# Performance work log

Hardware: AMD Instinct MI355X
Metric: run time of the kernel (lower is better)

The kernel has to match this reference:

```python
import jax, jax.numpy as jnp
import numpy as np

B, CIN, COUT, H, W, K = 4, 64, 64, 128, 128, 3
KK = K * K


def setup_inputs() -> dict:
    key = jax.random.key(0)
    k1, k2, k3, k4 = jax.random.split(key, 4)
    x = jax.random.normal(k1, (B, CIN, H, W), dtype=jnp.float32)
    offset = jax.random.normal(k2, (B, 2 * KK, H, W), dtype=jnp.float32)
    mask = jax.random.uniform(k3, (B, KK, H, W), dtype=jnp.float32)
    n = CIN * KK
    stdv = 1.0 / np.sqrt(n)
    weight = jax.random.uniform(k4, (COUT, CIN, K, K), dtype=jnp.float32,
                                minval=-stdv, maxval=stdv)
    bias = jnp.zeros((COUT,), dtype=jnp.float32)
    return {"x": x, "offset": offset, "mask": mask, "weight": weight, "bias": bias}


def _sample(x, ci, cj):
    # x: (b,c,h,w); ci,cj: (b,h,w,kk) int32 -> (b,c,h,w,kk), zero outside bounds
    b, c, h, w = x.shape
    valid = (ci >= 0) & (ci < h) & (cj >= 0) & (cj < w)  # (b,h,w,kk)
    idx = jnp.clip(ci, 0, h - 1) * w + jnp.clip(cj, 0, w - 1)
    flat = x.reshape(b, c, h * w)
    g = jnp.take_along_axis(flat, idx.reshape(b, 1, -1), axis=2)
    g = g.reshape(b, c, h, w, -1)
    return jnp.where(valid[:, None], g, jnp.zeros((), x.dtype))


def reference(x, offset, mask, weight, bias):
    b, c, h, w = x.shape
    # offset: (b, kk*2, h, w) -> (b, h, w, kk, 2)
    off = offset.reshape(b, KK, 2, h, w).transpose(0, 3, 4, 1, 2)
    # base sampling grid: coord[i,j,ki,kj] = (i-1+ki, j-1+kj), flattened over kk
    di, dj = jnp.meshgrid(jnp.arange(-(K // 2), K // 2 + 1),
                          jnp.arange(-(K // 2), K // 2 + 1), indexing='ij')
    base_i = jnp.arange(h, dtype=jnp.float32)[:, None, None] + di.reshape(1, 1, KK)
    base_j = jnp.arange(w, dtype=jnp.float32)[None, :, None] + dj.reshape(1, 1, KK)
    coord_i = off[..., 0] + base_i  # (b,h,w,kk)
    coord_j = off[..., 1] + base_j

    lt_i = jnp.floor(coord_i)
    lt_j = jnp.floor(coord_j)
    rb_i = jnp.ceil(coord_i)
    rb_j = jnp.ceil(coord_j)
    li, lj = lt_i.astype(jnp.int32), lt_j.astype(jnp.int32)
    ri, rj = rb_i.astype(jnp.int32), rb_j.astype(jnp.int32)

    v_lt = _sample(x, li, lj)
    v_rb = _sample(x, ri, rj)
    v_rt = _sample(x, li, rj)
    v_lb = _sample(x, ri, lj)

    # bilinear fractions, broadcast over channel dim
    fi = (coord_i - lt_i)[:, None]  # (b,1,h,w,kk)
    fj = (coord_j - lt_j)[:, None]
    v_t = v_lt + fj * (v_rt - v_lt)
    v_b = v_lb + fj * (v_rb - v_lb)
    v = v_t + fi * (v_b - v_t)  # (b,c,h,w,kk)

    # modulation mask: (b,kk,h,w) -> (b,1,h,w,kk)
    v = v * mask.transpose(0, 2, 3, 1)[:, None]

    w_flat = weight.reshape(weight.shape[0], c, KK)
    out = jnp.einsum('oik,bihwk->bohw', w_flat, v)
    return out + bias[None, :, None, None]
```

## Files before the change

kernel.cpp:

```cpp
#include <hip/hip_runtime.h>

#define B_   4
#define CIN  64
#define COUT 64
#define H_   128
#define W_   128
#define HW   (H_*W_)
#define KK   9
#define PIX  (B_*H_*W_)
#define R_   4
#define REG  16
#define NBLK 1024

typedef short bf16x8 __attribute__((ext_vector_type(8)));
typedef float f32x4  __attribute__((ext_vector_type(4)));
typedef float f32x2  __attribute__((ext_vector_type(2)));
typedef unsigned int u32;
typedef unsigned int u32x4 __attribute__((ext_vector_type(4)));

__device__ __forceinline__ unsigned short f2bf(float f) {
    unsigned int u = __float_as_uint(f);
    u = (u + 0x7FFFu + ((u >> 16) & 1u)) >> 16;
    return (unsigned short)u;
}

__global__ __launch_bounds__(256) void k_transpose(const float* __restrict__ x,
                                                   unsigned short* __restrict__ xt) {
    __shared__ float lds[64 * 129];
    int bi = blockIdx.x;
    int b = bi >> 7, i = bi & 127;
    int tid = threadIdx.x;
#pragma unroll
    for (int cc = 0; cc < 32; ++cc) {
        int c = cc * 2 + (tid >> 7);
        int w = tid & 127;
        lds[c * 129 + w] = x[((b * CIN + c) * H_ + i) * W_ + w];
    }
    __syncthreads();
#pragma unroll
    for (int q = 0; q < 32; ++q) {
        int c = tid & 63;
        int w = q * 4 + (tid >> 6);
        xt[((b * H_ + i) * W_ + w) * CIN + c] = f2bf(lds[c * 129 + w]);
    }
}

__global__ __launch_bounds__(256) void k_weight(const float* __restrict__ w,
                                                unsigned short* __restrict__ wtf) {
    int t = blockIdx.x * 256 + threadIdx.x;
    if (t >= 18 * 4 * 64 * 8) return;
    int j    = t & 7;
    int lane = (t >> 3) & 63;
    int nt   = (t >> 9) & 3;
    int s    = t >> 11;
    int kg   = s * 32 + ((lane >> 4) << 3) + j;
    int n    = nt * 16 + (lane & 15);
    int kpos = kg >> 6, c = kg & 63;
    wtf[t] = f2bf(w[(n * CIN + c) * 9 + kpos]);
}

__global__ __launch_bounds__(256, 4) void k_main(
    const unsigned short* __restrict__ xt,
    const float* __restrict__ offset,
    const float* __restrict__ mask,
    const unsigned short* __restrict__ wtf,
    const float* __restrict__ bias,
    float* __restrict__ out) {
    __shared__ __align__(16) unsigned char smem[REG * REG * 128];

    const int tid  = threadIdx.x;
    const int lane = tid & 63;
    const int wv   = tid >> 6;
    const int T  = ((blockIdx.x & 7) << 7) + (blockIdx.x >> 3);
    const int b  = T >> 8;
    const int i0 = ((T >> 4) & 15) * 8;
    const int j0 = (T & 15) * 8;
    const char* xb = (const char*)xt + (size_t)b * HW * 128;

    {
        const int iA = i0 - R_, jA = j0 - R_;
#pragma unroll
        for (int k = 0; k < 8; ++k) {
            int linear = k * 256 + tid;
            int rec = linear >> 3, c = linear & 7;
            int gr = min(max(iA + (rec >> 4), 0), H_ - 1);
            int gc = min(max(jA + (rec & 15), 0), W_ - 1);
            u32x4 v = *(const u32x4*)(xb + ((gr * W_ + gc) << 7) + (c << 4));
            *(u32x4*)(smem + (rec << 7) + (((c + rec) & 7) << 4)) = v;
        }
    }
    __syncthreads();

    const int p  = lane & 15;
    const int g  = lane >> 4;
    const int ir = i0 + wv * 2 + (p >> 3);
    const int jc = j0 + (p & 7);
    const float* offp = offset + (size_t)b * 18 * HW + ir * W_ + jc;
    const float* mskp = mask   + (size_t)b * 9  * HW + ir * W_ + jc;
    const bf16x8* wp  = (const bf16x8*)wtf;

    f32x4 acc0 = {0,0,0,0}, acc1 = {0,0,0,0}, acc2 = {0,0,0,0}, acc3 = {0,0,0,0};

#pragma unroll
    for (int kp = 0; kp < 9; ++kp) {
        float oi  = offp[(2 * kp) * HW];
        float oj  = offp[(2 * kp + 1) * HW];
        float msk = mskp[kp * HW];
        float ci = oi + (float)(ir + kp / 3 - 1);
        float cj = oj + (float)(jc + kp % 3 - 1);
        float fli = floorf(ci), flj = floorf(cj);
        float fi = ci - fli, fj = cj - flj;
        int li = (int)fli, lj = (int)flj;
        int li1 = li + 1, lj1 = lj + 1;
        float vy0 = (li  >= 0 && li  < H_) ? 1.f : 0.f;
        float vy1 = (li1 >= 0 && li1 < H_) ? 1.f : 0.f;
        float vx0 = (lj  >= 0 && lj  < W_) ? 1.f : 0.f;
        float vx1 = (lj1 >= 0 && lj1 < W_) ? 1.f : 0.f;
        float gi = fi * msk, gj = fj * msk;
        float w11 = gi * fj;
        f32x4 w4;
        w4.x = (msk - gi - gj + w11) * vy0 * vx0;
        w4.y = (gj - w11) * vy0 * vx1;
        w4.z = (gi - w11) * vy1 * vx0;
        w4.w = w11 * vy1 * vx1;
        int y0 = min(max(li,  0), H_ - 1), y1 = min(max(li1, 0), H_ - 1);
        int x0 = min(max(lj,  0), W_ - 1), x1 = min(max(lj1, 0), W_ - 1);
        int a00 = (y0 * W_ + x0) << 7, a01 = (y0 * W_ + x1) << 7;
        int a10 = (y1 * W_ + x0) << 7, a11 = (y1 * W_ + x1) << 7;
        int rli = li - (i0 - R_), rlj = lj - (j0 - R_);
        bool inr = ((unsigned)rli <= 14u) && ((unsigned)rlj <= 14u);
        int rli_c = min(max(rli, 0), 14), rlj_c = min(max(rlj, 0), 14);
        int r00 = rli_c * 16 + rlj_c;
        int r01 = r00 + 1, r10 = r00 + 16, r11 = r00 + 17;

#pragma unroll
        for (int h = 0; h < 2; ++h) {
            int ch = h * 4 + g;
            u32x4 q00 = *(const u32x4*)(smem + (r00 << 7) + (((ch + r00) & 7) << 4));
            u32x4 q01 = *(const u32x4*)(smem + (r01 << 7) + (((ch + r01) & 7) << 4));
            u32x4 q10 = *(const u32x4*)(smem + (r10 << 7) + (((ch + r10) & 7) << 4));
            u32x4 q11 = *(const u32x4*)(smem + (r11 << 7) + (((ch + r11) & 7) << 4));
            if (!inr) {
                int c = (g << 4) + (h << 6);
                q00 = *(const u32x4*)(xb + a00 + c);
                q01 = *(const u32x4*)(xb + a01 + c);
                q10 = *(const u32x4*)(xb + a10 + c);
                q11 = *(const u32x4*)(xb + a11 + c);
            }
            f32x2 wx = {w4.x, w4.x}, wy = {w4.y, w4.y};
            f32x2 wz = {w4.z, w4.z}, ww = {w4.w, w4.w};
            u32x4 po;
#pragma unroll
            for (int q = 0; q < 4; ++q) {
                f32x2 c00 = {__uint_as_float(q00[q] << 16), __uint_as_float(q00[q] & 0xFFFF0000u)};
                f32x2 c01 = {__uint_as_float(q01[q] << 16), __uint_as_float(q01[q] & 0xFFFF0000u)};
                f32x2 c10 = {__uint_as_float(q10[q] << 16), __uint_as_float(q10[q] & 0xFFFF0000u)};
                f32x2 c11 = {__uint_as_float(q11[q] << 16), __uint_as_float(q11[q] & 0xFFFF0000u)};
                f32x2 r = wx * c00 + wy * c01 + wz * c10 + ww * c11;
                po[q] = __builtin_amdgcn_perm(__float_as_uint(r.y) + 0x8000u,
                                              __float_as_uint(r.x) + 0x8000u, 0x07060302u);
            }
            bf16x8 af; *(u32x4*)&af = po;
            int s = kp * 2 + h;
            acc0 = __builtin_amdgcn_mfma_f32_16x16x32_bf16(af, wp[(s*4+0)*64 + lane], acc0, 0, 0, 0);
            acc1 = __builtin_amdgcn_mfma_f32_16x16x32_bf16(af, wp[(s*4+1)*64 + lane], acc1, 0, 0, 0);
            acc2 = __builtin_amdgcn_mfma_f32_16x16x32_bf16(af, wp[(s*4+2)*64 + lane], acc2, 0, 0, 0);
            acc3 = __builtin_amdgcn_mfma_f32_16x16x32_bf16(af, wp[(s*4+3)*64 + lane], acc3, 0, 0, 0);
        }
    }

    __syncthreads();
    float* cst = (float*)smem;
    {
        f32x4 v0 = acc0, v1 = acc1, v2 = acc2, v3 = acc3;
        float bs0 = bias[p], bs1 = bias[16 + p], bs2 = bias[32 + p], bs3 = bias[48 + p];
#pragma unroll
        for (int r = 0; r < 4; ++r) { v0[r] += bs0; v1[r] += bs1; v2[r] += bs2; v3[r] += bs3; }
        const int pm = wv * 16 + (g << 2);
        *(f32x4*)&cst[(p)      * 68 + pm] = v0;
        *(f32x4*)&cst[(16 + p) * 68 + pm] = v1;
        *(f32x4*)&cst[(32 + p) * 68 + pm] = v2;
        *(f32x4*)&cst[(48 + p) * 68 + pm] = v3;
    }
    __syncthreads();
    const int cl  = tid >> 4;
    const int px4 = (tid & 15) * 4;
    const size_t obase = (size_t)b * (COUT * HW) + (i0 + (px4 >> 3)) * W_ + j0 + (px4 & 7);
#pragma unroll
    for (int c4 = 0; c4 < 4; ++c4) {
        int cout = c4 * 16 + cl;
        f32x4 vv = *(const f32x4*)&cst[cout * 68 + px4];
        __builtin_nontemporal_store(vv, (f32x4*)&out[obase + (size_t)cout * HW]);
    }
}

extern "C" void kernel_launch(void* const* d_in, const int* in_sizes, int n_in,
                              void* d_out, int out_size, void* d_ws, size_t ws_size,
                              hipStream_t stream) {
    const float* x      = (const float*)d_in[0];
    const float* offset = (const float*)d_in[1];
    const float* mask   = (const float*)d_in[2];
    const float* weight = (const float*)d_in[3];
    const float* bias   = (const float*)d_in[4];
    float* out = (float*)d_out;
    unsigned short* xt  = (unsigned short*)d_ws;
    unsigned short* wtf = xt + (size_t)B_ * H_ * W_ * CIN;

    k_transpose<<<B_ * H_, 256, 0, stream>>>(x, xt);
    k_weight<<<144, 256, 0, stream>>>(weight, wtf);
    k_main<<<NBLK, 256, 0, stream>>>(xt, offset, mask, wtf, bias, out);
}
```

Baseline: 43.28 us.

## Enlarge output tile to 8x16 with 512 threads and stage offset/mask in LDS

Each block now covers an 8x16 pixel tile with 8 waves instead of 8x8 with 4 waves, so the halo region (16x24) is shared across more output pixels and less redundant halo data is loaded. Offset and mask values are staged into LDS with coalesced 16-byte loads rather than read per-lane from global memory. Output stores are also wider per row. This raises per-block LDS use (about 65KB) and thread count, which may lower occupancy.

```diff
diff --git a/kernel.cpp b/kernel.cpp
--- a/kernel.cpp
+++ b/kernel.cpp
@@ -7,10 +7,11 @@
 #define W_   128
 #define HW   (H_*W_)
 #define KK   9
-#define PIX  (B_*H_*W_)
-#define R_   4
-#define REG  16
-#define NBLK 1024
+#define ROWS_R 16
+#define COLS_R 24
+#define OFFB  (ROWS_R * COLS_R * 128)
+#define SMEMB (OFFB + 27 * 128 * 4)
+#define NBLK 512
 
 typedef short bf16x8 __attribute__((ext_vector_type(8)));
 typedef float f32x4  __attribute__((ext_vector_type(4)));
@@ -59,53 +60,73 @@
     wtf[t] = f2bf(w[(n * CIN + c) * 9 + kpos]);
 }
 
-__global__ __launch_bounds__(256, 4) void k_main(
+__global__ __launch_bounds__(512, 4) void k_main(
     const unsigned short* __restrict__ xt,
     const float* __restrict__ offset,
     const float* __restrict__ mask,
     const unsigned short* __restrict__ wtf,
     const float* __restrict__ bias,
     float* __restrict__ out) {
-    __shared__ __align__(16) unsigned char smem[REG * REG * 128];
+    __shared__ __align__(16) unsigned char smem[SMEMB];
 
     const int tid  = threadIdx.x;
     const int lane = tid & 63;
     const int wv   = tid >> 6;
-    const int T  = ((blockIdx.x & 7) << 7) + (blockIdx.x >> 3);
-    const int b  = T >> 8;
-    const int i0 = ((T >> 4) & 15) * 8;
-    const int j0 = (T & 15) * 8;
+    const int T  = ((blockIdx.x & 7) << 6) + (blockIdx.x >> 3);
+    const int b  = T >> 7;
+    const int i0 = ((T >> 3) & 15) * 8;
+    const int j0 = (T & 7) * 16;
     const char* xb = (const char*)xt + (size_t)b * HW * 128;
 
     {
-        const int iA = i0 - R_, jA = j0 - R_;
-#pragma unroll
-        for (int k = 0; k < 8; ++k) {
-            int linear = k * 256 + tid;
-            int rec = linear >> 3, c = linear & 7;
-            int gr = min(max(iA + (rec >> 4), 0), H_ - 1);
-            int gc = min(max(jA + (rec & 15), 0), W_ - 1);
-            u32x4 v = *(const u32x4*)(xb + ((gr * W_ + gc) << 7) + (c << 4));
+        const int iA = i0 - 4, jA = j0 - 4;
+#pragma unroll
+        for (int k = 0; k < 6; ++k) {
+            int idx = k * 512 + tid;
+            int rec = idx >> 3, c = idx & 7;
+            int rr = rec / COLS_R, cc = rec - rr * COLS_R;
+            int gr = min(max(iA + rr, 0), H_ - 1);
+            int gc = min(max(jA + cc, 0), W_ - 1);
+            u32x4 v = *(const u32x4*)(xb + (((gr << 7) + gc) << 7) + (c << 4));
             *(u32x4*)(smem + (rec << 7) + (((c + rec) & 7) << 4)) = v;
         }
     }
+    {
+        const float* op = offset + (size_t)b * 18 * HW;
+        const float* mp = mask   + (size_t)b * 9  * HW;
+#pragma unroll
+        for (int k = 0; k < 2; ++k) {
+            int idx = k * 512 + tid;
+            if (idx < 864) {
+                int q = idx >> 5, rem = idx & 31;
+                int row = rem >> 2, c4 = (rem & 3) << 2;
+                const float* src = (q < 18 ? op + q * HW : mp + (q - 18) * HW)
+                                   + (i0 + row) * W_ + j0 + c4;
+                *(f32x4*)(smem + OFFB + idx * 16) = *(const f32x4*)src;
+            }
+        }
+    }
     __syncthreads();
 
     const int p  = lane & 15;
     const int g  = lane >> 4;
-    const int ir = i0 + wv * 2 + (p >> 3);
-    const int jc = j0 + (p & 7);
-    const float* offp = offset + (size_t)b * 18 * HW + ir * W_ + jc;
-    const float* mskp = mask   + (size_t)b * 9  * HW + ir * W_ + jc;
-    const bf16x8* wp  = (const bf16x8*)wtf;
-
+    const int ir = i0 + wv;
+    const int jc = j0 + p;
+    const float* offl = (const float*)(smem + OFFB);
+    float offv[18], mskv[9];
+#pragma unroll
+    for (int q = 0; q < 18; ++q) offv[q] = offl[q * 128 + wv * 16 + p];
+#pragma unroll
+    for (int q = 0; q < 9; ++q)  mskv[q] = offl[(18 + q) * 128 + wv * 16 + p];
+
+    const bf16x8* wp = (const bf16x8*)wtf;
     f32x4 acc0 = {0,0,0,0}, acc1 = {0,0,0,0}, acc2 = {0,0,0,0}, acc3 = {0,0,0,0};
 
 #pragma unroll
     for (int kp = 0; kp < 9; ++kp) {
-        float oi  = offp[(2 * kp) * HW];
-        float oj  = offp[(2 * kp + 1) * HW];
-        float msk = mskp[kp * HW];
+        float oi  = offv[2 * kp];
+        float oj  = offv[2 * kp + 1];
+        float msk = mskv[kp];
         float ci = oi + (float)(ir + kp / 3 - 1);
         float cj = oj + (float)(jc + kp % 3 - 1);
         float fli = floorf(ci), flj = floorf(cj);
@@ -125,13 +146,14 @@
         w4.w = w11 * vy1 * vx1;
         int y0 = min(max(li,  0), H_ - 1), y1 = min(max(li1, 0), H_ - 1);
         int x0 = min(max(lj,  0), W_ - 1), x1 = min(max(lj1, 0), W_ - 1);
-        int a00 = (y0 * W_ + x0) << 7, a01 = (y0 * W_ + x1) << 7;
-        int a10 = (y1 * W_ + x0) << 7, a11 = (y1 * W_ + x1) << 7;
-        int rli = li - (i0 - R_), rlj = lj - (j0 - R_);
-        bool inr = ((unsigned)rli <= 14u) && ((unsigned)rlj <= 14u);
-        int rli_c = min(max(rli, 0), 14), rlj_c = min(max(rlj, 0), 14);
-        int r00 = rli_c * 16 + rlj_c;
-        int r01 = r00 + 1, r10 = r00 + 16, r11 = r00 + 17;
+        int a00 = ((y0 << 7) + x0) << 7, a01 = ((y0 << 7) + x1) << 7;
+        int a10 = ((y1 << 7) + x0) << 7, a11 = ((y1 << 7) + x1) << 7;
+        int rli = li - (i0 - 4), rlj = lj - (j0 - 4);
+        bool inr = ((unsigned)rli <= (unsigned)(ROWS_R - 2)) &&
+                   ((unsigned)rlj <= (unsigned)(COLS_R - 2));
+        int rli_c = min(max(rli, 0), ROWS_R - 2), rlj_c = min(max(rlj, 0), COLS_R - 2);
+        int r00 = rli_c * COLS_R + rlj_c;
+        int r01 = r00 + 1, r10 = r00 + COLS_R, r11 = r00 + COLS_R + 1;
 
 #pragma unroll
         for (int h = 0; h < 2; ++h) {
@@ -177,20 +199,21 @@
 #pragma unroll
         for (int r = 0; r < 4; ++r) { v0[r] += bs0; v1[r] += bs1; v2[r] += bs2; v3[r] += bs3; }
         const int pm = wv * 16 + (g << 2);
-        *(f32x4*)&cst[(p)      * 68 + pm] = v0;
-        *(f32x4*)&cst[(16 + p) * 68 + pm] = v1;
-        *(f32x4*)&cst[(32 + p) * 68 + pm] = v2;
-        *(f32x4*)&cst[(48 + p) * 68 + pm] = v3;
-    }
-    __syncthreads();
-    const int cl  = tid >> 4;
-    const int px4 = (tid & 15) * 4;
-    const size_t obase = (size_t)b * (COUT * HW) + (i0 + (px4 >> 3)) * W_ + j0 + (px4 & 7);
-#pragma unroll
-    for (int c4 = 0; c4 < 4; ++c4) {
-        int cout = c4 * 16 + cl;
-        f32x4 vv = *(const f32x4*)&cst[cout * 68 + px4];
-        __builtin_nontemporal_store(vv, (f32x4*)&out[obase + (size_t)cout * HW]);
+        *(f32x4*)&cst[(p)      * 132 + pm] = v0;
+        *(f32x4*)&cst[(16 + p) * 132 + pm] = v1;
+        *(f32x4*)&cst[(32 + p) * 132 + pm] = v2;
+        *(f32x4*)&cst[(48 + p) * 132 + pm] = v3;
+    }
+    __syncthreads();
+    const size_t obase = (size_t)b * (COUT * HW) + i0 * W_ + j0;
+#pragma unroll
+    for (int k = 0; k < 4; ++k) {
+        int idx = k * 512 + tid;
+        int cout = idx >> 5, chunk = idx & 31;
+        int row = chunk >> 2, col = (chunk & 3) << 2;
+        f32x4 vv = *(const f32x4*)&cst[cout * 132 + chunk * 4];
+        __builtin_nontemporal_store(vv,
+            (f32x4*)&out[obase + (size_t)cout * HW + row * W_ + col]);
     }
 }
 
@@ -208,5 +231,5 @@
 
     k_transpose<<<B_ * H_, 256, 0, stream>>>(x, xt);
     k_weight<<<144, 256, 0, stream>>>(weight, wtf);
-    k_main<<<NBLK, 256, 0, stream>>>(xt, offset, mask, wtf, bias, out);
-}
+    k_main<<<NBLK, 512, 0, stream>>>(xt, offset, mask, wtf, bias, out);
+}
```

Result: faster. 37.98 us (-12.2%).
